# Performance work log

Measured on AMD Instinct MI355X. Metric: run time of the kernel, lower is better.

Reference implementation:

```python
import jax, jax.numpy as jnp
import numpy as np
import math

B, T, D, H = 2, 2048, 1024, 16
HD = D // H
SOFTMAX_EPS = 1e-9
LN_EPS = 1e-5
NEG_INF = -1e9

def setup_inputs() -> dict:
    key = jax.random.key(0)
    ks = jax.random.split(key, 8)
    x = jax.random.normal(ks[0], (B, T, D), dtype=jnp.float32)
    # additive causal mask: 0 on/below diagonal, -1e9 above
    causal = jnp.where(jnp.tril(jnp.ones((T, T), dtype=bool)), 0.0, NEG_INF).astype(jnp.float32)
    attn_mask = jnp.broadcast_to(causal, (B, T, T))
    s = 0.02
    W_proj = jax.random.normal(ks[1], (D, 3 * D), dtype=jnp.float32) * s
    b_proj = jnp.zeros((3 * D,), dtype=jnp.float32)
    W_out = jax.random.normal(ks[2], (D, D), dtype=jnp.float32) * s
    b_out = jnp.zeros((D,), dtype=jnp.float32)
    ln_gamma = jnp.ones((D,), dtype=jnp.float32)
    ln_beta = jnp.zeros((D,), dtype=jnp.float32)
    return {"x": x, "attn_mask": attn_mask, "W_proj": W_proj, "b_proj": b_proj,
            "W_out": W_out, "b_out": b_out, "ln_gamma": ln_gamma, "ln_beta": ln_beta}

def reference(x, attn_mask, W_proj, b_proj, W_out, b_out, ln_gamma, ln_beta):
    Bv, Tv = x.shape[0], x.shape[1]
    qkv = x @ W_proj + b_proj                      # [B,T,3D]
    q, k, v = jnp.split(qkv, 3, axis=-1)
    q = q.reshape(Bv, Tv, H, HD).transpose(0, 2, 1, 3)  # [B,H,T,hd]
    k = k.reshape(Bv, Tv, H, HD).transpose(0, 2, 1, 3)
    v = v.reshape(Bv, Tv, H, HD).transpose(0, 2, 1, 3)
    # NOTE: mask added BEFORE scaling, matching the original module
    scores = (jnp.einsum('bhqd,bhkd->bhqk', q, k) + attn_mask[:, None, :, :]) / math.sqrt(HD)
    num = jnp.exp(scores)
    wts = num / (num.sum(axis=-1, keepdims=True) + SOFTMAX_EPS)  # eps-safe softmax, no max-subtract
    attn = jnp.einsum('bhqk,bhkd->bhqd', wts, v)   # [B,H,T,hd]
    y = attn.transpose(0, 2, 1, 3).reshape(Bv, Tv, D)
    z = x + y @ W_out + b_out
    mu = z.mean(axis=-1, keepdims=True)
    var = ((z - mu) ** 2).mean(axis=-1, keepdims=True)
    return (z - mu) / jnp.sqrt(var + LN_EPS) * ln_gamma + ln_beta
```

## Files before the change

kernel.cpp:

```cpp
#include <hip/hip_runtime.h>
#include <stdint.h>

typedef unsigned short u16;
typedef __attribute__((ext_vector_type(8))) short short8;
typedef __attribute__((ext_vector_type(4))) short sh4;
typedef __attribute__((ext_vector_type(4))) float f32x4;

#define MFMA16(a,b,c) __builtin_amdgcn_mfma_f32_16x16x32_bf16((a),(b),(c),0,0,0)

__device__ __forceinline__ u16 f2bf(float f) {
  union { float f; uint32_t u; } c; c.f = f;
  uint32_t u = c.u;
  return (u16)((u + 0x7fffu + ((u >> 16) & 1u)) >> 16);
}

__device__ __forceinline__ float fast_exp2(float x) {
#if __has_builtin(__builtin_amdgcn_exp2f)
  return __builtin_amdgcn_exp2f(x);
#else
  return __expf(x * 0.69314718056f);
#endif
}

__device__ __forceinline__ void async_cp16(const void* g, void* l) {
  __builtin_amdgcn_global_load_lds((__attribute__((address_space(1))) void*)g,
                                   (__attribute__((address_space(3))) void*)l,
                                   16, 0, 0);
}

__global__ __launch_bounds__(256) void prep(const float* __restrict__ x,
                                            const float* __restrict__ Wp,
                                            const float* __restrict__ Wo,
                                            u16* __restrict__ x_bf,
                                            u16* __restrict__ WpT,
                                            u16* __restrict__ WoT) {
  int bx = blockIdx.x;
  int t = threadIdx.x;
  if (bx < 4096) {
    int i = bx * 256 + t;
    float4 v = ((const float4*)x)[i];
    ushort4 o; o.x = f2bf(v.x); o.y = f2bf(v.y); o.z = f2bf(v.z); o.w = f2bf(v.w);
    ((ushort4*)x_bf)[i] = o;
    return;
  }
  __shared__ float tile[64][65];
  const float* in; u16* out; int C, blk;
  blk = bx - 4096;
  if (blk < 768) { in = Wp; out = WpT; C = 3072; }
  else           { in = Wo; out = WoT; C = 1024; blk -= 768; }
  const int R = 1024;
  int nbc = C >> 6;
  int c0 = (blk % nbc) << 6;
  int r0 = (blk / nbc) << 6;
  int li = t & 15;
  int hi = t >> 4;
  for (int i = 0; i < 4; i++) {
    int r = hi + (i << 4);
    float4 v = *(const float4*)&in[(size_t)(r0 + r) * C + c0 + (li << 2)];
    tile[r][(li << 2) + 0] = v.x;
    tile[r][(li << 2) + 1] = v.y;
    tile[r][(li << 2) + 2] = v.z;
    tile[r][(li << 2) + 3] = v.w;
  }
  __syncthreads();
  int rr4 = li << 2;
  for (int i = 0; i < 4; i++) {
    int col = hi + (i << 4);
    ushort4 o;
    o.x = f2bf(tile[rr4 + 0][col]);
    o.y = f2bf(tile[rr4 + 1][col]);
    o.z = f2bf(tile[rr4 + 2][col]);
    o.w = f2bf(tile[rr4 + 3][col]);
    *(ushort4*)&out[(size_t)(c0 + col) * R + r0 + rr4] = o;
  }
}

__global__ __launch_bounds__(256, 2) void gemm_qkv(
    const u16* __restrict__ A, const u16* __restrict__ Bt,
    const float* __restrict__ bias, u16* __restrict__ qkb, u16* __restrict__ Vtb) {
  __shared__ __align__(16) u16 As[8192];
  __shared__ __align__(16) u16 Bs[4096];
  int t = threadIdx.x;
  int w = t >> 6, lane = t & 63, quad = lane >> 4, l15 = lane & 15;
  int wr = w >> 1, wc = w & 1;
  int m0 = blockIdx.y * 128;
  int n0 = blockIdx.x * 64;
  bool isqk = (n0 < 2048);

  const u16* gA[4]; u16* lA[4];
  const u16* gB[2]; u16* lB[2];
  {
    int rbase = t >> 2, cg = t & 3;
    for (int i = 0; i < 4; i++) {
      int r = rbase + (i & 1) * 64;
      int half = i >> 1;
      gA[i] = A + (size_t)(m0 + r) * 1024 + half * 32 + cg * 8;
      lA[i] = &As[half * 4096 + r * 32 + cg * 8];
    }
    for (int i = 0; i < 2; i++) {
      gB[i] = Bt + (size_t)(n0 + rbase) * 1024 + i * 32 + cg * 8;
      lB[i] = &Bs[i * 2048 + rbase * 32 + cg * 8];
    }
  }

  f32x4 acc[4][2];
  f32x4 zero = {0.f, 0.f, 0.f, 0.f};
  for (int mt = 0; mt < 4; mt++)
    for (int nt = 0; nt < 2; nt++) acc[mt][nt] = zero;

  for (int k0 = 0; k0 < 1024; k0 += 64) {
    __syncthreads();
    for (int i = 0; i < 4; i++) async_cp16(gA[i] + k0, lA[i]);
    for (int i = 0; i < 2; i++) async_cp16(gB[i] + k0, lB[i]);
    __syncthreads();
    for (int kc = 0; kc < 2; kc++) {
      short8 af[4], bf[2];
      for (int mt = 0; mt < 4; mt++)
        af[mt] = *(const short8*)&As[kc * 4096 + (wr * 64 + mt * 16 + l15) * 32 + quad * 8];
      for (int nt = 0; nt < 2; nt++)
        bf[nt] = *(const short8*)&Bs[kc * 2048 + (wc * 32 + nt * 16 + l15) * 32 + quad * 8];
      if (isqk) {
        for (int mt = 0; mt < 4; mt++)
          for (int nt = 0; nt < 2; nt++)
            acc[mt][nt] = MFMA16(bf[nt], af[mt], acc[mt][nt]);
      } else {
        for (int mt = 0; mt < 4; mt++)
          for (int nt = 0; nt < 2; nt++)
            acc[mt][nt] = MFMA16(af[mt], bf[nt], acc[mt][nt]);
      }
    }
  }
  if (isqk) {
    float qscale = (n0 < 1024) ? 0.18033688011112042f : 1.0f;
    for (int mt = 0; mt < 4; mt++) {
      int m = m0 + wr * 64 + mt * 16 + l15;
      for (int nt = 0; nt < 2; nt++) {
        int nb = n0 + wc * 32 + nt * 16 + quad * 4;
        float4 bv = *(const float4*)&bias[nb];
        ushort4 o;
        o.x = f2bf((acc[mt][nt][0] + bv.x) * qscale);
        o.y = f2bf((acc[mt][nt][1] + bv.y) * qscale);
        o.z = f2bf((acc[mt][nt][2] + bv.z) * qscale);
        o.w = f2bf((acc[mt][nt][3] + bv.w) * qscale);
        *(ushort4*)&qkb[(size_t)m * 2048 + nb] = o;
      }
    }
  } else {
    for (int nt = 0; nt < 2; nt++) {
      int n = n0 + wc * 32 + nt * 16 + l15;
      float bv = bias[n];
      int d = n - 2048;
      for (int mt = 0; mt < 4; mt++) {
        int mb = m0 + wr * 64 + mt * 16 + quad * 4;
        ushort4 o;
        o.x = f2bf(acc[mt][nt][0] + bv);
        o.y = f2bf(acc[mt][nt][1] + bv);
        o.z = f2bf(acc[mt][nt][2] + bv);
        o.w = f2bf(acc[mt][nt][3] + bv);
        *(ushort4*)&Vtb[(size_t)d * 4096 + mb] = o;
      }
    }
  }
}

__global__ __launch_bounds__(256, 2) void gemm_out_res(
    const u16* __restrict__ A, const u16* __restrict__ Bt,
    const float* __restrict__ bias, const float* __restrict__ X,
    float* __restrict__ Z) {
  __shared__ __align__(16) u16 As[8192];
  __shared__ __align__(16) u16 Bs[4096];
  int t = threadIdx.x;
  int w = t >> 6, lane = t & 63, quad = lane >> 4, l15 = lane & 15;
  int wr = w >> 1, wc = w & 1;
  int m0 = blockIdx.y * 128;
  int n0 = blockIdx.x * 64;

  const u16* gA[4]; u16* lA[4];
  const u16* gB[2]; u16* lB[2];
  {
    int rbase = t >> 2, cg = t & 3;
    for (int i = 0; i < 4; i++) {
      int r = rbase + (i & 1) * 64;
      int half = i >> 1;
      gA[i] = A + (size_t)(m0 + r) * 1024 + half * 32 + cg * 8;
      lA[i] = &As[half * 4096 + r * 32 + cg * 8];
    }
    for (int i = 0; i < 2; i++) {
      gB[i] = Bt + (size_t)(n0 + rbase) * 1024 + i * 32 + cg * 8;
      lB[i] = &Bs[i * 2048 + rbase * 32 + cg * 8];
    }
  }

  f32x4 acc[4][2];
  f32x4 zero = {0.f, 0.f, 0.f, 0.f};
  for (int mt = 0; mt < 4; mt++)
    for (int nt = 0; nt < 2; nt++) acc[mt][nt] = zero;

  for (int k0 = 0; k0 < 1024; k0 += 64) {
    __syncthreads();
    for (int i = 0; i < 4; i++) async_cp16(gA[i] + k0, lA[i]);
    for (int i = 0; i < 2; i++) async_cp16(gB[i] + k0, lB[i]);
    __syncthreads();
    for (int kc = 0; kc < 2; kc++) {
      short8 af[4], bf[2];
      for (int mt = 0; mt < 4; mt++)
        af[mt] = *(const short8*)&As[kc * 4096 + (wr * 64 + mt * 16 + l15) * 32 + quad * 8];
      for (int nt = 0; nt < 2; nt++)
        bf[nt] = *(const short8*)&Bs[kc * 2048 + (wc * 32 + nt * 16 + l15) * 32 + quad * 8];
      for (int mt = 0; mt < 4; mt++)
        for (int nt = 0; nt < 2; nt++)
          acc[mt][nt] = MFMA16(bf[nt], af[mt], acc[mt][nt]);
    }
  }
  for (int mt = 0; mt < 4; mt++) {
    int m = m0 + wr * 64 + mt * 16 + l15;
    for (int nt = 0; nt < 2; nt++) {
      int nb = n0 + wc * 32 + nt * 16 + quad * 4;
      float4 bv = *(const float4*)&bias[nb];
      size_t idx = (size_t)m * 1024 + nb;
      float4 xv = *(const float4*)&X[idx];
      float4 o;
      o.x = acc[mt][nt][0] + bv.x + xv.x;
      o.y = acc[mt][nt][1] + bv.y + xv.y;
      o.z = acc[mt][nt][2] + bv.z + xv.z;
      o.w = acc[mt][nt][3] + bv.w + xv.w;
      *(float4*)&Z[idx] = o;
    }
  }
}

#define LDPK 72
__global__ __launch_bounds__(256, 2) void attn_v6(
    const u16* __restrict__ qk, const u16* __restrict__ Vt,
    u16* __restrict__ y) {
  __shared__ __align__(16) u16 K_lds[2][4096];
  __shared__ __align__(16) u16 V_lds[2][4096];
  __shared__ __align__(16) u16 P_lds[4 * 16 * LDPK];
  __shared__ float rs_sh[4][16];
  int bx = blockIdx.x;
  int bh = bx & 31;
  int qt = 31 - (bx >> 5);
  int h = bh & 15, b = bh >> 4;
  int t = threadIdx.x, w = t >> 6, lane = t & 63, quad = lane >> 4, l15 = lane & 15;
  size_t rowbase = (size_t)b * 2048;
  u16* Pw = P_lds + w * 16 * LDPK;
  f32x4 zero = {0.f, 0.f, 0.f, 0.f};

  const u16 *Kg[2], *Vg[2];
  u16 *Kl[2][2], *Vl[2][2];
  for (int i = 0; i < 2; i++) {
    int c = t + 256 * i;
    int half = c >> 8, row = (c >> 2) & 63, cg = c & 3;
    int col = half * 32 + cg * 8;
    Kg[i] = qk + (rowbase + row) * 2048 + 1024 + h * 64 + col;
    Vg[i] = Vt + (size_t)(h * 64 + row) * 4096 + rowbase + col;
    Kl[0][i] = &K_lds[0][c * 8]; Kl[1][i] = &K_lds[1][c * 8];
    Vl[0][i] = &V_lds[0][c * 8]; Vl[1][i] = &V_lds[1][c * 8];
  }

  for (int i = 0; i < 2; i++) { async_cp16(Kg[i], Kl[0][i]); async_cp16(Vg[i], Vl[0][i]); }

  int cur = 0;
  int q0 = qt * 64;
  short8 qf0, qf1;
  {
    const u16* qp = qk + (rowbase + q0 + w * 16 + l15) * 2048 + h * 64 + quad * 8;
    qf0 = *(const short8*)qp;
    qf1 = *(const short8*)(qp + 32);
  }
  f32x4 o[4];
  for (int nt = 0; nt < 4; nt++) o[nt] = zero;
  float rsl = 0.f;

  for (int kt = 0; kt <= qt; kt++) {
    __syncthreads();
    int nxt = cur ^ 1;
    if (kt < qt) {
      size_t ko = (size_t)(kt + 1) * 64;
      for (int i = 0; i < 2; i++) {
        async_cp16(Kg[i] + ko * 2048, Kl[nxt][i]);
        async_cp16(Vg[i] + ko, Vl[nxt][i]);
      }
    }
    const u16* Kb = K_lds[cur];
    const u16* Vb = V_lds[cur];
    f32x4 s[4];
    for (int nt = 0; nt < 4; nt++) {
      const u16* kr = Kb + (nt * 16 + l15) * 32 + quad * 8;
      f32x4 a2 = zero;
      a2 = MFMA16(*(const short8*)kr, qf0, a2);
      a2 = MFMA16(*(const short8*)(kr + 2048), qf1, a2);
      s[nt] = a2;
    }
    bool diag = (kt == qt);
    int qg = w * 16 + l15;
    for (int nt = 0; nt < 4; nt++) {
      int kl = nt * 16 + quad * 4;
      float p0 = fast_exp2(s[nt][0]);
      float p1 = fast_exp2(s[nt][1]);
      float p2 = fast_exp2(s[nt][2]);
      float p3 = fast_exp2(s[nt][3]);
      if (diag) {
        if (kl + 0 > qg) p0 = 0.f;
        if (kl + 1 > qg) p1 = 0.f;
        if (kl + 2 > qg) p2 = 0.f;
        if (kl + 3 > qg) p3 = 0.f;
      }
      rsl += (p0 + p1) + (p2 + p3);
      uint32_t w0 = __builtin_amdgcn_perm(__float_as_uint(p1), __float_as_uint(p0), 0x07060302u);
      uint32_t w1 = __builtin_amdgcn_perm(__float_as_uint(p3), __float_as_uint(p2), 0x07060302u);
      uint2 pk; pk.x = w0; pk.y = w1;
      *(uint2*)&Pw[l15 * LDPK + kl] = pk;
    }
    for (int c2 = 0; c2 < 2; c2++) {
      short8 af = *(const short8*)&Pw[l15 * LDPK + c2 * 32 + quad * 8];
      for (int nt = 0; nt < 4; nt++) {
        const short8 bv = *(const short8*)&Vb[c2 * 2048 + (nt * 16 + l15) * 32 + quad * 8];
        o[nt] = MFMA16(af, bv, o[nt]);
      }
    }
    cur = nxt;
  }
  rsl += __shfl_xor(rsl, 16, 64);
  rsl += __shfl_xor(rsl, 32, 64);
  if (lane < 16) rs_sh[w][lane] = rsl;
  float rq[4];
  for (int r = 0; r < 4; r++) rq[r] = rs_sh[w][quad * 4 + r] + 1e-9f;
  for (int nt = 0; nt < 4; nt++) {
    for (int r = 0; r < 4; r++) {
      float ov = o[nt][r] / rq[r];
      size_t qr = rowbase + q0 + w * 16 + quad * 4 + r;
      y[qr * 1024 + h * 64 + nt * 16 + l15] = f2bf(ov);
    }
  }
}

__global__ __launch_bounds__(256) void ln_kernel(const float* __restrict__ Z,
                                                 const float* __restrict__ gamma,
                                                 const float* __restrict__ beta,
                                                 float* __restrict__ out) {
  int row = blockIdx.x;
  int t = threadIdx.x;
  float4 v = ((const float4*)(Z + (size_t)row * 1024))[t];
  float s = v.x + v.y + v.z + v.w;
  float s2 = v.x * v.x + v.y * v.y + v.z * v.z + v.w * v.w;
  for (int m = 1; m < 64; m <<= 1) {
    s += __shfl_xor(s, m, 64);
    s2 += __shfl_xor(s2, m, 64);
  }
  __shared__ float ss[4], ss2[4];
  int w = t >> 6;
  if ((t & 63) == 0) { ss[w] = s; ss2[w] = s2; }
  __syncthreads();
  s = ss[0] + ss[1] + ss[2] + ss[3];
  s2 = ss2[0] + ss2[1] + ss2[2] + ss2[3];
  float mu = s * (1.0f / 1024.0f);
  float var = s2 * (1.0f / 1024.0f) - mu * mu;
  float inv = rsqrtf(var + 1e-5f);
  float4 g = ((const float4*)gamma)[t];
  float4 bb = ((const float4*)beta)[t];
  float4 o;
  o.x = (v.x - mu) * inv * g.x + bb.x;
  o.y = (v.y - mu) * inv * g.y + bb.y;
  o.z = (v.z - mu) * inv * g.z + bb.z;
  o.w = (v.w - mu) * inv * g.w + bb.w;
  ((float4*)(out + (size_t)row * 1024))[t] = o;
}

extern "C" void kernel_launch(void* const* d_in, const int* in_sizes, int n_in,
                              void* d_out, int out_size, void* d_ws, size_t ws_size,
                              hipStream_t stream) {
  const float* x     = (const float*)d_in[0];
  const float* Wp    = (const float*)d_in[2];
  const float* bp    = (const float*)d_in[3];
  const float* Wo    = (const float*)d_in[4];
  const float* bo    = (const float*)d_in[5];
  const float* gamma = (const float*)d_in[6];
  const float* beta  = (const float*)d_in[7];
  float* out = (float*)d_out;

  char* ws = (char*)d_ws;
  u16*   x_bf = (u16*)(ws);
  u16*   WpT  = (u16*)(ws + 8388608);
  u16*   WoT  = (u16*)(ws + 14680064);
  u16*   qkb  = (u16*)(ws + 16777216);
  u16*   Vtb  = (u16*)(ws + 33554432);
  u16*   y    = (u16*)(ws + 41943040);
  float* z    = (float*)(ws + 50331648);

  prep<<<5120, 256, 0, stream>>>(x, Wp, Wo, x_bf, WpT, WoT);

  dim3 gqkv(48, 32);
  gemm_qkv<<<gqkv, 256, 0, stream>>>(x_bf, WpT, bp, qkb, Vtb);

  attn_v6<<<1024, 256, 0, stream>>>(qkb, Vtb, y);

  dim3 go(16, 32);
  gemm_out_res<<<go, 256, 0, stream>>>(y, WoT, bo, x, z);

  ln_kernel<<<4096, 256, 0, stream>>>(z, gamma, beta, out);
}
```

Baseline: 209.4 us.

## Switch projection GEMMs to 32x32x16 MFMA and widen QKV tile to 128x128

Both projection GEMMs now use the 32x32x16 bf16 MFMA instead of 16x16x32, which lowers LDS fragment loads per FLOP. The QKV GEMM tile also grows from 128x64 to 128x128 per block, halving its grid and the number of times A tiles are re-read. Epilogues are rewritten for the 32x32 accumulator layout. The trade-off is fewer blocks (768 for QKV) and more accumulator registers per thread.

```diff
diff --git a/kernel.cpp b/kernel.cpp
--- a/kernel.cpp
+++ b/kernel.cpp
@@ -5,8 +5,10 @@
 typedef __attribute__((ext_vector_type(8))) short short8;
 typedef __attribute__((ext_vector_type(4))) short sh4;
 typedef __attribute__((ext_vector_type(4))) float f32x4;
+typedef __attribute__((ext_vector_type(16))) float f32x16;
 
 #define MFMA16(a,b,c) __builtin_amdgcn_mfma_f32_16x16x32_bf16((a),(b),(c),0,0,0)
+#define MFMA32(a,b,c) __builtin_amdgcn_mfma_f32_32x32x16_bf16((a),(b),(c),0,0,0)
 
 __device__ __forceinline__ u16 f2bf(float f) {
   union { float f; uint32_t u; } c; c.f = f;
@@ -78,14 +80,107 @@
 __global__ __launch_bounds__(256, 2) void gemm_qkv(
     const u16* __restrict__ A, const u16* __restrict__ Bt,
     const float* __restrict__ bias, u16* __restrict__ qkb, u16* __restrict__ Vtb) {
-  __shared__ __align__(16) u16 As[8192];
-  __shared__ __align__(16) u16 Bs[4096];
+  __shared__ __align__(16) u16 As[2][4096];
+  __shared__ __align__(16) u16 Bs[2][4096];
   int t = threadIdx.x;
-  int w = t >> 6, lane = t & 63, quad = lane >> 4, l15 = lane & 15;
+  int w = t >> 6, lane = t & 63, l31 = lane & 31, lh = lane >> 5;
+  int wr = w >> 1, wc = w & 1;
+  int m0 = blockIdx.y * 128;
+  int n0 = blockIdx.x * 128;
+  bool isqk = (n0 < 2048);
+
+  const u16* gA[4]; u16* lA[4];
+  const u16* gB[4]; u16* lB[4];
+  {
+    int rbase = t >> 2, cg = t & 3;
+    for (int i = 0; i < 4; i++) {
+      int r = rbase + (i & 1) * 64;
+      int half = i >> 1;
+      gA[i] = A + (size_t)(m0 + r) * 1024 + half * 32 + cg * 8;
+      gB[i] = Bt + (size_t)(n0 + r) * 1024 + half * 32 + cg * 8;
+      lA[i] = &As[half][r * 32 + cg * 8];
+      lB[i] = &Bs[half][r * 32 + cg * 8];
+    }
+  }
+
+  f32x16 acc[2][2];
+  for (int mt = 0; mt < 2; mt++)
+    for (int nt = 0; nt < 2; nt++)
+      for (int j = 0; j < 16; j++) acc[mt][nt][j] = 0.f;
+
+  for (int k0 = 0; k0 < 1024; k0 += 64) {
+    __syncthreads();
+    for (int i = 0; i < 4; i++) {
+      async_cp16(gA[i] + k0, lA[i]);
+      async_cp16(gB[i] + k0, lB[i]);
+    }
+    __syncthreads();
+    for (int s = 0; s < 4; s++) {
+      int pl = s >> 1, ko = (s & 1) * 16 + lh * 8;
+      short8 af[2], bf[2];
+      for (int mt = 0; mt < 2; mt++)
+        af[mt] = *(const short8*)&As[pl][(wr * 64 + mt * 32 + l31) * 32 + ko];
+      for (int nt = 0; nt < 2; nt++)
+        bf[nt] = *(const short8*)&Bs[pl][(wc * 64 + nt * 32 + l31) * 32 + ko];
+      if (isqk) {
+        for (int mt = 0; mt < 2; mt++)
+          for (int nt = 0; nt < 2; nt++)
+            acc[mt][nt] = MFMA32(bf[nt], af[mt], acc[mt][nt]);
+      } else {
+        for (int mt = 0; mt < 2; mt++)
+          for (int nt = 0; nt < 2; nt++)
+            acc[mt][nt] = MFMA32(af[mt], bf[nt], acc[mt][nt]);
+      }
+    }
+  }
+  if (isqk) {
+    float qscale = (n0 < 1024) ? 0.18033688011112042f : 1.0f;
+    for (int mt = 0; mt < 2; mt++) {
+      int m = m0 + wr * 64 + mt * 32 + l31;
+      for (int nt = 0; nt < 2; nt++) {
+        for (int g = 0; g < 4; g++) {
+          int nb = n0 + wc * 64 + nt * 32 + 4 * lh + 8 * g;
+          float4 bv = *(const float4*)&bias[nb];
+          ushort4 o;
+          o.x = f2bf((acc[mt][nt][4 * g + 0] + bv.x) * qscale);
+          o.y = f2bf((acc[mt][nt][4 * g + 1] + bv.y) * qscale);
+          o.z = f2bf((acc[mt][nt][4 * g + 2] + bv.z) * qscale);
+          o.w = f2bf((acc[mt][nt][4 * g + 3] + bv.w) * qscale);
+          *(ushort4*)&qkb[(size_t)m * 2048 + nb] = o;
+        }
+      }
+    }
+  } else {
+    for (int nt = 0; nt < 2; nt++) {
+      int n = n0 + wc * 64 + nt * 32 + l31;
+      float bv = bias[n];
+      int d = n - 2048;
+      for (int mt = 0; mt < 2; mt++) {
+        for (int g = 0; g < 4; g++) {
+          int mb = m0 + wr * 64 + mt * 32 + 4 * lh + 8 * g;
+          ushort4 o;
+          o.x = f2bf(acc[mt][nt][4 * g + 0] + bv);
+          o.y = f2bf(acc[mt][nt][4 * g + 1] + bv);
+          o.z = f2bf(acc[mt][nt][4 * g + 2] + bv);
+          o.w = f2bf(acc[mt][nt][4 * g + 3] + bv);
+          *(ushort4*)&Vtb[(size_t)d * 4096 + mb] = o;
+        }
+      }
+    }
+  }
+}
+
+__global__ __launch_bounds__(256, 2) void gemm_out_res(
+    const u16* __restrict__ A, const u16* __restrict__ Bt,
+    const float* __restrict__ bias, const float* __restrict__ X,
+    float* __restrict__ Z) {
+  __shared__ __align__(16) u16 As[2][4096];
+  __shared__ __align__(16) u16 Bs[2][2048];
+  int t = threadIdx.x;
+  int w = t >> 6, lane = t & 63, l31 = lane & 31, lh = lane >> 5;
   int wr = w >> 1, wc = w & 1;
   int m0 = blockIdx.y * 128;
   int n0 = blockIdx.x * 64;
-  bool isqk = (n0 < 2048);
 
   const u16* gA[4]; u16* lA[4];
   const u16* gB[2]; u16* lB[2];
@@ -95,135 +190,45 @@
       int r = rbase + (i & 1) * 64;
       int half = i >> 1;
       gA[i] = A + (size_t)(m0 + r) * 1024 + half * 32 + cg * 8;
-      lA[i] = &As[half * 4096 + r * 32 + cg * 8];
+      lA[i] = &As[half][r * 32 + cg * 8];
     }
     for (int i = 0; i < 2; i++) {
       gB[i] = Bt + (size_t)(n0 + rbase) * 1024 + i * 32 + cg * 8;
-      lB[i] = &Bs[i * 2048 + rbase * 32 + cg * 8];
-    }
-  }
-
-  f32x4 acc[4][2];
-  f32x4 zero = {0.f, 0.f, 0.f, 0.f};
-  for (int mt = 0; mt < 4; mt++)
-    for (int nt = 0; nt < 2; nt++) acc[mt][nt] = zero;
+      lB[i] = &Bs[i][rbase * 32 + cg * 8];
+    }
+  }
+
+  f32x16 acc[2];
+  for (int mt = 0; mt < 2; mt++)
+    for (int j = 0; j < 16; j++) acc[mt][j] = 0.f;
 
   for (int k0 = 0; k0 < 1024; k0 += 64) {
     __syncthreads();
     for (int i = 0; i < 4; i++) async_cp16(gA[i] + k0, lA[i]);
     for (int i = 0; i < 2; i++) async_cp16(gB[i] + k0, lB[i]);
     __syncthreads();
-    for (int kc = 0; kc < 2; kc++) {
-      short8 af[4], bf[2];
-      for (int mt = 0; mt < 4; mt++)
-        af[mt] = *(const short8*)&As[kc * 4096 + (wr * 64 + mt * 16 + l15) * 32 + quad * 8];
-      for (int nt = 0; nt < 2; nt++)
-        bf[nt] = *(const short8*)&Bs[kc * 2048 + (wc * 32 + nt * 16 + l15) * 32 + quad * 8];
-      if (isqk) {
-        for (int mt = 0; mt < 4; mt++)
-          for (int nt = 0; nt < 2; nt++)
-            acc[mt][nt] = MFMA16(bf[nt], af[mt], acc[mt][nt]);
-      } else {
-        for (int mt = 0; mt < 4; mt++)
-          for (int nt = 0; nt < 2; nt++)
-            acc[mt][nt] = MFMA16(af[mt], bf[nt], acc[mt][nt]);
-      }
-    }
-  }
-  if (isqk) {
-    float qscale = (n0 < 1024) ? 0.18033688011112042f : 1.0f;
-    for (int mt = 0; mt < 4; mt++) {
-      int m = m0 + wr * 64 + mt * 16 + l15;
-      for (int nt = 0; nt < 2; nt++) {
-        int nb = n0 + wc * 32 + nt * 16 + quad * 4;
-        float4 bv = *(const float4*)&bias[nb];
-        ushort4 o;
-        o.x = f2bf((acc[mt][nt][0] + bv.x) * qscale);
-        o.y = f2bf((acc[mt][nt][1] + bv.y) * qscale);
-        o.z = f2bf((acc[mt][nt][2] + bv.z) * qscale);
-        o.w = f2bf((acc[mt][nt][3] + bv.w) * qscale);
-        *(ushort4*)&qkb[(size_t)m * 2048 + nb] = o;
-      }
-    }
-  } else {
-    for (int nt = 0; nt < 2; nt++) {
-      int n = n0 + wc * 32 + nt * 16 + l15;
-      float bv = bias[n];
-      int d = n - 2048;
-      for (int mt = 0; mt < 4; mt++) {
-        int mb = m0 + wr * 64 + mt * 16 + quad * 4;
-        ushort4 o;
-        o.x = f2bf(acc[mt][nt][0] + bv);
-        o.y = f2bf(acc[mt][nt][1] + bv);
-        o.z = f2bf(acc[mt][nt][2] + bv);
-        o.w = f2bf(acc[mt][nt][3] + bv);
-        *(ushort4*)&Vtb[(size_t)d * 4096 + mb] = o;
-      }
-    }
-  }
-}
-
-__global__ __launch_bounds__(256, 2) void gemm_out_res(
-    const u16* __restrict__ A, const u16* __restrict__ Bt,
-    const float* __restrict__ bias, const float* __restrict__ X,
-    float* __restrict__ Z) {
-  __shared__ __align__(16) u16 As[8192];
-  __shared__ __align__(16) u16 Bs[4096];
-  int t = threadIdx.x;
-  int w = t >> 6, lane = t & 63, quad = lane >> 4, l15 = lane & 15;
-  int wr = w >> 1, wc = w & 1;
-  int m0 = blockIdx.y * 128;
-  int n0 = blockIdx.x * 64;
-
-  const u16* gA[4]; u16* lA[4];
-  const u16* gB[2]; u16* lB[2];
-  {
-    int rbase = t >> 2, cg = t & 3;
-    for (int i = 0; i < 4; i++) {
-      int r = rbase + (i & 1) * 64;
-      int half = i >> 1;
-      gA[i] = A + (size_t)(m0 + r) * 1024 + half * 32 + cg * 8;
-      lA[i] = &As[half * 4096 + r * 32 + cg * 8];
-    }
-    for (int i = 0; i < 2; i++) {
-      gB[i] = Bt + (size_t)(n0 + rbase) * 1024 + i * 32 + cg * 8;
-      lB[i] = &Bs[i * 2048 + rbase * 32 + cg * 8];
-    }
-  }
-
-  f32x4 acc[4][2];
-  f32x4 zero = {0.f, 0.f, 0.f, 0.f};
-  for (int mt = 0; mt < 4; mt++)
-    for (int nt = 0; nt < 2; nt++) acc[mt][nt] = zero;
-
-  for (int k0 = 0; k0 < 1024; k0 += 64) {
-    __syncthreads();
-    for (int i = 0; i < 4; i++) async_cp16(gA[i] + k0, lA[i]);
-    for (int i = 0; i < 2; i++) async_cp16(gB[i] + k0, lB[i]);
-    __syncthreads();
-    for (int kc = 0; kc < 2; kc++) {
-      short8 af[4], bf[2];
-      for (int mt = 0; mt < 4; mt++)
-        af[mt] = *(const short8*)&As[kc * 4096 + (wr * 64 + mt * 16 + l15) * 32 + quad * 8];
-      for (int nt = 0; nt < 2; nt++)
-        bf[nt] = *(const short8*)&Bs[kc * 2048 + (wc * 32 + nt * 16 + l15) * 32 + quad * 8];
-      for (int mt = 0; mt < 4; mt++)
-        for (int nt = 0; nt < 2; nt++)
-          acc[mt][nt] = MFMA16(bf[nt], af[mt], acc[mt][nt]);
-    }
-  }
-  for (int mt = 0; mt < 4; mt++) {
-    int m = m0 + wr * 64 + mt * 16 + l15;
-    for (int nt = 0; nt < 2; nt++) {
-      int nb = n0 + wc * 32 + nt * 16 + quad * 4;
+    for (int s = 0; s < 4; s++) {
+      int pl = s >> 1, ko = (s & 1) * 16 + lh * 8;
+      short8 af[2], bf;
+      for (int mt = 0; mt < 2; mt++)
+        af[mt] = *(const short8*)&As[pl][(wr * 64 + mt * 32 + l31) * 32 + ko];
+      bf = *(const short8*)&Bs[pl][(wc * 32 + l31) * 32 + ko];
+      for (int mt = 0; mt < 2; mt++)
+        acc[mt] = MFMA32(bf, af[mt], acc[mt]);
+    }
+  }
+  for (int mt = 0; mt < 2; mt++) {
+    int m = m0 + wr * 64 + mt * 32 + l31;
+    for (int g = 0; g < 4; g++) {
+      int nb = n0 + wc * 32 + 4 * lh + 8 * g;
       float4 bv = *(const float4*)&bias[nb];
       size_t idx = (size_t)m * 1024 + nb;
       float4 xv = *(const float4*)&X[idx];
       float4 o;
-      o.x = acc[mt][nt][0] + bv.x + xv.x;
-      o.y = acc[mt][nt][1] + bv.y + xv.y;
-      o.z = acc[mt][nt][2] + bv.z + xv.z;
-      o.w = acc[mt][nt][3] + bv.w + xv.w;
+      o.x = acc[mt][4 * g + 0] + bv.x + xv.x;
+      o.y = acc[mt][4 * g + 1] + bv.y + xv.y;
+      o.z = acc[mt][4 * g + 2] + bv.z + xv.z;
+      o.w = acc[mt][4 * g + 3] + bv.w + xv.w;
       *(float4*)&Z[idx] = o;
     }
   }
@@ -390,7 +395,7 @@
 
   prep<<<5120, 256, 0, stream>>>(x, Wp, Wo, x_bf, WpT, WoT);
 
-  dim3 gqkv(48, 32);
+  dim3 gqkv(24, 32);
   gemm_qkv<<<gqkv, 256, 0, stream>>>(x_bf, WpT, bp, qkb, Vtb);
 
   attn_v6<<<1024, 256, 0, stream>>>(qkb, Vtb, y);
```

Result: no change. 213.1 us (+1.8%).
